# Kernel optimization log

Hardware: AMD Instinct MI355X
Metric: run time of the kernel (lower is better)

Reference implementation:

```python
import jax, jax.numpy as jnp
import numpy as np

D = 768

def _linear_params(key, name_idx, d_in, d_out):
    k1, k2 = jax.random.split(jax.random.fold_in(jax.random.key(42), name_idx))
    bound = 1.0 / np.sqrt(d_in)
    W = jax.random.uniform(k1, (d_out, d_in), jnp.float32, -bound, bound)
    b = jax.random.uniform(k2, (d_out,), jnp.float32, -bound, bound)
    return W, b

def setup_inputs() -> dict:
    key = jax.random.key(0)
    kq, kk, kv = jax.random.split(key, 3)
    B, S = 8, 2048
    inp = {
        'query': jax.random.normal(kq, (B, S, D), jnp.float32),
        'key': jax.random.normal(kk, (B, S, D), jnp.float32),
        'value': jax.random.normal(kv, (B, S, D), jnp.float32),
    }
    Wq, bq = _linear_params(key, 0, D, D)
    Wk, bk = _linear_params(key, 1, D, D)
    Wv, bv = _linear_params(key, 2, D, D)
    Wg1, bg1 = _linear_params(key, 3, D, D)
    Wg2, bg2 = _linear_params(key, 4, D, D)
    inp.update(Wq=Wq, bq=bq, Wk=Wk, bk=bk, Wv=Wv, bv=bv,
               Wg1=Wg1, bg1=bg1, Wg2=Wg2, bg2=bg2,
               text_scale=jnp.ones((1, D), jnp.float32))
    return inp

def reference(query, key, value, Wq, bq, Wk, bk, Wv, bv, Wg1, bg1, Wg2, bg2, text_scale):
    # Linear projections (torch Linear: x @ W.T + b)
    q = jnp.einsum('bsd,ed->bse', query, Wq) + bq
    k = jnp.einsum('bsd,ed->bse', key, Wk) + bk
    v = jnp.einsum('bsd,ed->bse', value, Wv) + bv
    scale = 1.0 / jnp.sqrt(jnp.float32(k.shape[-1]))
    scores = jnp.einsum('bqd,bkd->bqk', q, k) * scale  # [B, S, S]
    attn = jax.nn.softmax(scores, axis=-1)
    attended = jnp.einsum('bqk,bkd->bqd', attn, v)  # dropout = identity (eval)
    # text_gate: Linear -> ReLU -> Linear -> Sigmoid, then sigmoid applied AGAIN (faithful)
    h = jax.nn.relu(jnp.einsum('bsd,ed->bse', attended, Wg1) + bg1)
    gate = jax.nn.sigmoid(jnp.einsum('bsd,ed->bse', h, Wg2) + bg2)
    gated = jax.nn.sigmoid(gate) * attended * text_scale
    return gated
```

## Files before the change

kernel.cpp:

```cpp
#include <hip/hip_runtime.h>

typedef unsigned short ushort_t;
typedef __bf16 bf16x8 __attribute__((ext_vector_type(8)));
typedef float f32x4 __attribute__((ext_vector_type(4)));
typedef short short8 __attribute__((ext_vector_type(8)));

#define SBAR()   asm volatile("s_barrier" ::: "memory")
#define WAITV0() asm volatile("s_waitcnt vmcnt(0)" ::: "memory")
#define WAITV4() asm volatile("s_waitcnt vmcnt(4)" ::: "memory")
#define WAITV8() asm volatile("s_waitcnt vmcnt(8)" ::: "memory")

__device__ __forceinline__ float bf2f(unsigned short u) {
    union { unsigned int i; float f; } v; v.i = ((unsigned int)u) << 16; return v.f;
}
__device__ __forceinline__ unsigned short f2bf(float f) {
    union { float f; unsigned int i; } v; v.f = f;
    unsigned int r = v.i + 0x7fffu + ((v.i >> 16) & 1u);
    return (unsigned short)(r >> 16);
}
__device__ __forceinline__ float sigm(float x) { return 1.0f / (1.0f + __expf(-x)); }

__device__ __forceinline__ void async_copy16(const ushort_t* src, ushort_t* dst_lds) {
    __builtin_amdgcn_global_load_lds(
        (const __attribute__((address_space(1))) void*)src,
        (__attribute__((address_space(3))) void*)dst_lds,
        16, 0, 0);
}

#define WSEG 589824
#define NWALL 2949120
#define NTOT 2953728
__global__ __launch_bounds__(256)
void convert_params(const float* __restrict__ Wq, const float* __restrict__ Wk,
                    const float* __restrict__ Wv, const float* __restrict__ Wg1,
                    const float* __restrict__ Wg2, const float* __restrict__ bq,
                    const float* __restrict__ bk, const float* __restrict__ bv,
                    const float* __restrict__ bg1, const float* __restrict__ bg2,
                    const float* __restrict__ ts, ushort_t* __restrict__ dst)
{
    int i = (blockIdx.x * 256 + threadIdx.x) * 8;
    if (i >= NTOT) return;
    const float* src; int off;
    if (i < NWALL) {
        int wi = i / WSEG; off = i - wi * WSEG;
        src = (wi == 0) ? Wq : (wi == 1) ? Wk : (wi == 2) ? Wv : (wi == 3) ? Wg1 : Wg2;
    } else {
        int j = i - NWALL; int bi = j / 768; off = j - bi * 768;
        src = (bi == 0) ? bq : (bi == 1) ? bk : (bi == 2) ? bv : (bi == 3) ? bg1 : (bi == 4) ? bg2 : ts;
    }
    float4 a = *(const float4*)(src + off);
    float4 b = *(const float4*)(src + off + 4);
    short8 o;
    o[0] = (short)f2bf(a.x); o[1] = (short)f2bf(a.y); o[2] = (short)f2bf(a.z); o[3] = (short)f2bf(a.w);
    o[4] = (short)f2bf(b.x); o[5] = (short)f2bf(b.y); o[6] = (short)f2bf(b.z); o[7] = (short)f2bf(b.w);
    *(short8*)(dst + i) = o;
}

#define PERT 12582912ll
__global__ __launch_bounds__(256)
void convert_inputs(const float* __restrict__ q, const float* __restrict__ k,
                    const float* __restrict__ v, ushort_t* __restrict__ X)
{
    long long i = ((long long)blockIdx.x * 256 + threadIdx.x) * 8;
    const float* src; long long off;
    if (i < PERT)          { src = q; off = i; }
    else if (i < 2 * PERT) { src = k; off = i - PERT; }
    else                   { src = v; off = i - 2 * PERT; }
    float4 a = *(const float4*)(src + off);
    float4 b = *(const float4*)(src + off + 4);
    short8 o;
    o[0] = (short)f2bf(a.x); o[1] = (short)f2bf(a.y); o[2] = (short)f2bf(a.z); o[3] = (short)f2bf(a.w);
    o[4] = (short)f2bf(b.x); o[5] = (short)f2bf(b.y); o[6] = (short)f2bf(b.z); o[7] = (short)f2bf(b.w);
    *(short8*)(X + i) = o;
}

__global__ __launch_bounds__(256)
void finalize_rinv(const float* __restrict__ psums, float* __restrict__ rinv, int nb)
{
    int row = blockIdx.x * 256 + threadIdx.x;
    const float* p = psums + (size_t)row * nb;
    float s = 0.f;
    for (int i = 0; i < nb; ++i) s += p[i];
    rinv[row] = 1.0f / s;
}

template<int EPI, int CF32, int QKV>
__global__ __launch_bounds__(256, 2)
void gemm_bt(const ushort_t* __restrict__ A, const ushort_t* __restrict__ B,
             void* __restrict__ Cv, void* __restrict__ Cv2,
             const ushort_t* __restrict__ bias,
             const ushort_t* __restrict__ aux, const ushort_t* __restrict__ ts,
             const float* __restrict__ rinvg, float* __restrict__ psum_out,
             int M, int N, int K, float scale,
             long long batchA, long long batchB, long long batchC)
{
    __shared__ __align__(16) ushort_t As[3][128 * 32];
    __shared__ __align__(16) ushort_t Bs[3][128 * 32];
    __shared__ float rsmx[256];
    const int tid  = threadIdx.x;
    const int lane = tid & 63;
    const int wave = tid >> 6;
    const int wr = wave >> 1, wc = wave & 1;

    const int gx = gridDim.x, gy = gridDim.y;
    const int nwg = gx * gy * gridDim.z;
    int fid = (blockIdx.z * gy + blockIdx.y) * gx + blockIdx.x;
    fid = (fid & 7) * (nwg >> 3) + (fid >> 3);
    const int bz  = fid / (gx * gy);
    const int rem = fid - bz * (gx * gy);
    const int by  = rem / gx;
    const int bx  = rem - by * gx;
    const int row0 = by * 128;
    const int col0 = bx * 128;

    f32x4 acc[4][4] = {};

    const int srow = tid >> 2;
    const int scol = (tid & 3) * 8;
    const ushort_t* ga0 = A + batchA * bz + (size_t)(row0 + srow) * K + scol;
    const ushort_t* gb0 = B + batchB * bz + (size_t)(col0 + srow) * K + scol;

    const int kop  = (lane >> 4) * 8;
    const int arow = wr * 64 + (lane & 15);
    const int brow = wc * 64 + (lane & 15);

    const int NT = K >> 5;

#define STAGE4(T, BUF) do { const int kk_ = (T) * 32; \
    async_copy16(ga0 + kk_,                  &As[BUF][0] + tid * 8); \
    async_copy16(ga0 + (size_t)64 * K + kk_, &As[BUF][0] + 2048 + tid * 8); \
    async_copy16(gb0 + kk_,                  &Bs[BUF][0] + tid * 8); \
    async_copy16(gb0 + (size_t)64 * K + kk_, &Bs[BUF][0] + 2048 + tid * 8); \
} while (0)

    STAGE4(0, 0);
    STAGE4(1, 1);

    int cur = 0;
    for (int t = 0; t < NT; ++t) {
        if (t + 2 < NT) {
            int nb = cur + 2; if (nb >= 3) nb -= 3;
            STAGE4(t + 2, nb);
            WAITV8();
        } else if (t + 1 < NT) {
            WAITV4();
        } else {
            WAITV0();
        }
        SBAR();
        const ushort_t* Ac = &As[0][0] + cur * 4096;
        const ushort_t* Bc = &Bs[0][0] + cur * 4096;
        bf16x8 af[4], bfr[4];
        #pragma unroll
        for (int m = 0; m < 4; ++m)
            af[m] = *(const bf16x8*)(Ac + (arow + m * 16) * 32 + kop);
        #pragma unroll
        for (int n = 0; n < 4; ++n)
            bfr[n] = *(const bf16x8*)(Bc + (brow + n * 16) * 32 + kop);
        #pragma unroll
        for (int m = 0; m < 4; ++m)
            #pragma unroll
            for (int n = 0; n < 4; ++n)
                acc[m][n] = __builtin_amdgcn_mfma_f32_16x16x32_bf16(af[m], bfr[n], acc[m][n], 0, 0, 0);
        SBAR();
        ++cur; if (cur >= 3) cur = 0;
    }
#undef STAGE4

    const int r0 = row0 + wr * 64 + (lane >> 4) * 4;
    const int c0 = col0 + wc * 64 + (lane & 15);

    float rv[4][4];
    if (EPI == 7) {
        #pragma unroll
        for (int m = 0; m < 4; ++m)
            #pragma unroll
            for (int r = 0; r < 4; ++r)
                rv[m][r] = rinvg[(size_t)bz * M + r0 + m * 16 + r];
    }
    float rsum[4][4] = {};

    ushort_t* Cb = (QKV && bz == 2) ? (ushort_t*)Cv2 : (ushort_t*)Cv + batchC * bz;
    float* Cf = (float*)Cv;
    #pragma unroll
    for (int m = 0; m < 4; ++m) {
        #pragma unroll
        for (int n = 0; n < 4; ++n) {
            const int col = c0 + n * 16;
            #pragma unroll
            for (int r = 0; r < 4; ++r) {
                const int row = r0 + m * 16 + r;
                float val = acc[m][n][r];
                if (EPI == 1) {
                    val += bf2f(bias[(QKV ? bz * 768 : 0) + col]);
                } else if (EPI == 3) {
                    val += bf2f(bias[col]);
                    val = fmaxf(val, 0.0f);
                } else if (EPI == 4) {
                    val += bf2f(bias[col]);
                    float g  = sigm(val);
                    float gg = sigm(g);
                    val = gg * bf2f(aux[(size_t)row * N + col]) * bf2f(ts[col]);
                } else if (EPI == 5) {
                    val = __expf(val * scale);
                    rsum[m][r] += val;
                } else if (EPI == 7) {
                    val *= rv[m][r];
                }
                if (CF32) Cf[(size_t)row * N + col] = val;
                else      Cb[(size_t)row * N + col] = f2bf(val);
            }
        }
    }

    if (EPI == 5) {
        #pragma unroll
        for (int m = 0; m < 4; ++m)
            #pragma unroll
            for (int r = 0; r < 4; ++r) {
                float s = rsum[m][r];
                s += __shfl_xor(s, 1);
                s += __shfl_xor(s, 2);
                s += __shfl_xor(s, 4);
                s += __shfl_xor(s, 8);
                rsum[m][r] = s;
            }
        if ((lane & 15) == 0) {
            const int quad = lane >> 4;
            #pragma unroll
            for (int m = 0; m < 4; ++m)
                #pragma unroll
                for (int r = 0; r < 4; ++r)
                    rsmx[(wr * 64 + m * 16 + quad * 4 + r) * 2 + wc] = rsum[m][r];
        }
        __syncthreads();
        if (tid < 128) {
            float s = rsmx[tid * 2] + rsmx[tid * 2 + 1];
            psum_out[((size_t)bz * M + row0 + tid) * gx + bx] = s;
        }
    }
}

__global__ __launch_bounds__(256)
void transpose2d(const ushort_t* __restrict__ V, ushort_t* __restrict__ VT, int R, int Ccols)
{
    __shared__ ushort_t t[32][33];
    const size_t zoff = (size_t)blockIdx.z * R * Ccols;
    const int tx = threadIdx.x, ty = threadIdx.y;
    const int c = blockIdx.x * 32 + tx;
    const int rbase = blockIdx.y * 32;
    #pragma unroll
    for (int i = 0; i < 4; ++i)
        t[ty + i * 8][tx] = V[zoff + (size_t)(rbase + ty + i * 8) * Ccols + c];
    __syncthreads();
    const int r = rbase + tx;
    const int cbase = blockIdx.x * 32;
    #pragma unroll
    for (int i = 0; i < 4; ++i)
        VT[zoff + (size_t)(cbase + ty + i * 8) * R + r] = t[tx][ty + i * 8];
}

extern "C" void kernel_launch(void* const* d_in, const int* in_sizes, int n_in,
                              void* d_out, int out_size, void* d_ws, size_t ws_size,
                              hipStream_t stream)
{
    (void)in_sizes; (void)n_in; (void)out_size; (void)ws_size;
    const float* query = (const float*)d_in[0];
    const float* key_  = (const float*)d_in[1];
    const float* value = (const float*)d_in[2];
    const float* Wq  = (const float*)d_in[3];
    const float* bq  = (const float*)d_in[4];
    const float* Wk  = (const float*)d_in[5];
    const float* bk  = (const float*)d_in[6];
    const float* Wv  = (const float*)d_in[7];
    const float* bv  = (const float*)d_in[8];
    const float* Wg1 = (const float*)d_in[9];
    const float* bg1 = (const float*)d_in[10];
    const float* Wg2 = (const float*)d_in[11];
    const float* bg2 = (const float*)d_in[12];
    const float* tsc = (const float*)d_in[13];

    const int S = 2048, D = 768, Bc = 8;
    const int MS = Bc * S;
    const long long SD = (long long)S * D;
    const long long SS = (long long)S * S;
    const long long MSD = (long long)MS * D;

    char* ws = (char*)d_ws;
    ushort_t* q    = (ushort_t*)(ws);
    ushort_t* att  = q;
    ushort_t* k    = (ushort_t*)(ws + 25165824ll);
    float*    rinv = (float*)(ws + 25165824ll);
    ushort_t* h    = k;
    ushort_t* vT   = (ushort_t*)(ws + 50331648ll);
    ushort_t* X    = (ushort_t*)(ws + 50331648ll);
    ushort_t* P    = (ushort_t*)(ws + 75497472ll);
    ushort_t* Wb   = (ushort_t*)(ws + 142606336ll);
    ushort_t* v    = (ushort_t*)d_out;
    float*  psums  = (float*)d_out;

    const int WQ = 0, WG1 = 1769472, WG2 = 2359296;
    const int BQ = 2949120, BG1 = 2951424, BG2 = 2952192, TSO = 2952960;

    const dim3 blk(256);
    const float scale = 0.03608439182435161f;

    convert_params<<<dim3((NTOT / 8 + 255) / 256), blk, 0, stream>>>(
        Wq, Wk, Wv, Wg1, Wg2, bq, bk, bv, bg1, bg2, tsc, Wb);
    convert_inputs<<<dim3(18432), blk, 0, stream>>>(query, key_, value, X);
    gemm_bt<1, 0, 1><<<dim3(D / 128, MS / 128, 3), blk, 0, stream>>>(
        X, Wb + WQ, q, v, Wb + BQ, nullptr, nullptr, nullptr, nullptr,
        MS, D, D, 1.f, MSD, (long long)WSEG, MSD);
    transpose2d<<<dim3(D / 32, S / 32, Bc), dim3(32, 8), 0, stream>>>(v, vT, S, D);
    gemm_bt<5, 0, 0><<<dim3(S / 128, S / 128, Bc), blk, 0, stream>>>(
        q, k, P, nullptr, nullptr, nullptr, nullptr, nullptr, psums,
        S, S, D, scale, SD, SD, SS);
    finalize_rinv<<<dim3(MS / 256), blk, 0, stream>>>(psums, rinv, S / 128);
    gemm_bt<7, 0, 0><<<dim3(D / 128, S / 128, Bc), blk, 0, stream>>>(
        P, vT, att, nullptr, nullptr, nullptr, nullptr, rinv, nullptr,
        S, D, S, 1.f, SS, SD, SD);
    gemm_bt<3, 0, 0><<<dim3(D / 128, MS / 128, 1), blk, 0, stream>>>(
        att, Wb + WG1, h, nullptr, Wb + BG1, nullptr, nullptr, nullptr, nullptr,
        MS, D, D, 1.f, 0, 0, 0);
    gemm_bt<4, 1, 0><<<dim3(D / 128, MS / 128, 1), blk, 0, stream>>>(
        h, Wb + WG2, d_out, nullptr, Wb + BG2, att, Wb + TSO, nullptr, nullptr,
        MS, D, D, 1.f, 0, 0, 0);
}
```

Baseline: 332.3 us.

## Fuse fp32-to-bf16 input conversion into QKV projection GEMM A-tile loading

Removes the separate convert_inputs kernel. The QKV GEMM now reads fp32 query/key/value directly, converts them to bf16 in registers and writes them into a double-buffered LDS A tile, while B tiles keep using async LDS copies. This avoids writing and re-reading a 75MB bf16 intermediate, at the cost of a more serialized A-load path with register prefetch and extra barriers. The float-to-bf16 conversion also switches to hardware casts.

```diff
diff --git a/kernel.cpp b/kernel.cpp
--- a/kernel.cpp
+++ b/kernel.cpp
@@ -8,7 +8,9 @@
 #define SBAR()   asm volatile("s_barrier" ::: "memory")
 #define WAITV0() asm volatile("s_waitcnt vmcnt(0)" ::: "memory")
 #define WAITV4() asm volatile("s_waitcnt vmcnt(4)" ::: "memory")
+#define WAITV6() asm volatile("s_waitcnt vmcnt(6)" ::: "memory")
 #define WAITV8() asm volatile("s_waitcnt vmcnt(8)" ::: "memory")
+#define WAITL0() asm volatile("s_waitcnt lgkmcnt(0)" ::: "memory")
 
 __device__ __forceinline__ float bf2f(unsigned short u) {
     union { unsigned int i; float f; } v; v.i = ((unsigned int)u) << 16; return v.f;
@@ -25,6 +27,13 @@
         (const __attribute__((address_space(1))) void*)src,
         (__attribute__((address_space(3))) void*)dst_lds,
         16, 0, 0);
+}
+
+__device__ __forceinline__ short8 cvt8(float4 x, float4 y) {
+    bf16x8 h;
+    h[0] = (__bf16)x.x; h[1] = (__bf16)x.y; h[2] = (__bf16)x.z; h[3] = (__bf16)x.w;
+    h[4] = (__bf16)y.x; h[5] = (__bf16)y.y; h[6] = (__bf16)y.z; h[7] = (__bf16)y.w;
+    return __builtin_bit_cast(short8, h);
 }
 
 #define WSEG 589824
@@ -50,28 +59,7 @@
     }
     float4 a = *(const float4*)(src + off);
     float4 b = *(const float4*)(src + off + 4);
-    short8 o;
-    o[0] = (short)f2bf(a.x); o[1] = (short)f2bf(a.y); o[2] = (short)f2bf(a.z); o[3] = (short)f2bf(a.w);
-    o[4] = (short)f2bf(b.x); o[5] = (short)f2bf(b.y); o[6] = (short)f2bf(b.z); o[7] = (short)f2bf(b.w);
-    *(short8*)(dst + i) = o;
-}
-
-#define PERT 12582912ll
-__global__ __launch_bounds__(256)
-void convert_inputs(const float* __restrict__ q, const float* __restrict__ k,
-                    const float* __restrict__ v, ushort_t* __restrict__ X)
-{
-    long long i = ((long long)blockIdx.x * 256 + threadIdx.x) * 8;
-    const float* src; long long off;
-    if (i < PERT)          { src = q; off = i; }
-    else if (i < 2 * PERT) { src = k; off = i - PERT; }
-    else                   { src = v; off = i - 2 * PERT; }
-    float4 a = *(const float4*)(src + off);
-    float4 b = *(const float4*)(src + off + 4);
-    short8 o;
-    o[0] = (short)f2bf(a.x); o[1] = (short)f2bf(a.y); o[2] = (short)f2bf(a.z); o[3] = (short)f2bf(a.w);
-    o[4] = (short)f2bf(b.x); o[5] = (short)f2bf(b.y); o[6] = (short)f2bf(b.z); o[7] = (short)f2bf(b.w);
-    *(short8*)(X + i) = o;
+    *(short8*)(dst + i) = cvt8(a, b);
 }
 
 __global__ __launch_bounds__(256)
@@ -84,9 +72,10 @@
     rinv[row] = 1.0f / s;
 }
 
-template<int EPI, int CF32, int QKV>
+template<int EPI, int CF32, int QKV, int AF32>
 __global__ __launch_bounds__(256, 2)
-void gemm_bt(const ushort_t* __restrict__ A, const ushort_t* __restrict__ B,
+void gemm_bt(const void* __restrict__ Av, const void* __restrict__ Af1,
+             const void* __restrict__ Af2, const ushort_t* __restrict__ B,
              void* __restrict__ Cv, void* __restrict__ Cv2,
              const ushort_t* __restrict__ bias,
              const ushort_t* __restrict__ aux, const ushort_t* __restrict__ ts,
@@ -117,7 +106,7 @@
 
     const int srow = tid >> 2;
     const int scol = (tid & 3) * 8;
-    const ushort_t* ga0 = A + batchA * bz + (size_t)(row0 + srow) * K + scol;
+    const ushort_t* ga0 = (const ushort_t*)Av + batchA * bz + (size_t)(row0 + srow) * K + scol;
     const ushort_t* gb0 = B + batchB * bz + (size_t)(col0 + srow) * K + scol;
 
     const int kop  = (lane >> 4) * 8;
@@ -126,6 +115,70 @@
 
     const int NT = K >> 5;
 
+#define MFMA_STEP(AC, BC) do { \
+    bf16x8 af_[4], bf_[4]; \
+    _Pragma("unroll") \
+    for (int m = 0; m < 4; ++m) af_[m] = *(const bf16x8*)((AC) + (arow + m * 16) * 32 + kop); \
+    _Pragma("unroll") \
+    for (int n = 0; n < 4; ++n) bf_[n] = *(const bf16x8*)((BC) + (brow + n * 16) * 32 + kop); \
+    _Pragma("unroll") \
+    for (int m = 0; m < 4; ++m) \
+        _Pragma("unroll") \
+        for (int n = 0; n < 4; ++n) \
+            acc[m][n] = __builtin_amdgcn_mfma_f32_16x16x32_bf16(af_[m], bf_[n], acc[m][n], 0, 0, 0); \
+} while (0)
+
+    if (AF32) {
+        const float* gAf = (bz == 0) ? (const float*)Av : (bz == 1) ? (const float*)Af1
+                                                        : (const float*)Af2;
+        const float* gA  = gAf + (size_t)(row0 + srow) * K + scol;
+        const float* gA2 = gA + (size_t)64 * K;
+
+#define STAGEB2(T, BUF) do { const int kk_ = (T) * 32; \
+    async_copy16(gb0 + kk_,                  &Bs[BUF][0] + tid * 8); \
+    async_copy16(gb0 + (size_t)64 * K + kk_, &Bs[BUF][0] + 2048 + tid * 8); } while (0)
+
+        STAGEB2(0, 0);
+        STAGEB2(1, 1);
+        float4 pa0 = *(const float4*)(gA);      float4 pa1 = *(const float4*)(gA + 4);
+        float4 pa2 = *(const float4*)(gA2);     float4 pa3 = *(const float4*)(gA2 + 4);
+        float4 qa0, qa1, qa2, qa3;
+
+        for (int t = 0; t < NT; t += 2) {
+            if (t + 2 < NT) STAGEB2(t + 2, (t + 2) % 3);
+            if (t + 1 < NT) {
+                const int k1 = (t + 1) * 32;
+                qa0 = *(const float4*)(gA + k1);  qa1 = *(const float4*)(gA + k1 + 4);
+                qa2 = *(const float4*)(gA2 + k1); qa3 = *(const float4*)(gA2 + k1 + 4);
+            }
+            if (t + 2 < NT)      WAITV6();
+            else if (t + 1 < NT) WAITV4();
+            else                 WAITV0();
+            *(short8*)(&As[0][0] + tid * 8)        = cvt8(pa0, pa1);
+            *(short8*)(&As[0][0] + 2048 + tid * 8) = cvt8(pa2, pa3);
+            WAITL0();
+            SBAR();
+            MFMA_STEP(&As[0][0], &Bs[0][0] + (t % 3) * 4096);
+            SBAR();
+            const int t1 = t + 1;
+            if (t1 + 2 < NT) STAGEB2(t1 + 2, (t1 + 2) % 3);
+            if (t1 + 1 < NT) {
+                const int k1 = (t1 + 1) * 32;
+                pa0 = *(const float4*)(gA + k1);  pa1 = *(const float4*)(gA + k1 + 4);
+                pa2 = *(const float4*)(gA2 + k1); pa3 = *(const float4*)(gA2 + k1 + 4);
+            }
+            if (t1 + 2 < NT)      WAITV6();
+            else if (t1 + 1 < NT) WAITV4();
+            else                  WAITV0();
+            *(short8*)(&As[1][0] + tid * 8)        = cvt8(qa0, qa1);
+            *(short8*)(&As[1][0] + 2048 + tid * 8) = cvt8(qa2, qa3);
+            WAITL0();
+            SBAR();
+            MFMA_STEP(&As[1][0], &Bs[0][0] + (t1 % 3) * 4096);
+            SBAR();
+        }
+#undef STAGEB2
+    } else {
 #define STAGE4(T, BUF) do { const int kk_ = (T) * 32; \
     async_copy16(ga0 + kk_,                  &As[BUF][0] + tid * 8); \
     async_copy16(ga0 + (size_t)64 * K + kk_, &As[BUF][0] + 2048 + tid * 8); \
@@ -133,39 +186,28 @@
     async_copy16(gb0 + (size_t)64 * K + kk_, &Bs[BUF][0] + 2048 + tid * 8); \
 } while (0)
 
-    STAGE4(0, 0);
-    STAGE4(1, 1);
-
-    int cur = 0;
-    for (int t = 0; t < NT; ++t) {
-        if (t + 2 < NT) {
-            int nb = cur + 2; if (nb >= 3) nb -= 3;
-            STAGE4(t + 2, nb);
-            WAITV8();
-        } else if (t + 1 < NT) {
-            WAITV4();
-        } else {
-            WAITV0();
-        }
-        SBAR();
-        const ushort_t* Ac = &As[0][0] + cur * 4096;
-        const ushort_t* Bc = &Bs[0][0] + cur * 4096;
-        bf16x8 af[4], bfr[4];
-        #pragma unroll
-        for (int m = 0; m < 4; ++m)
-            af[m] = *(const bf16x8*)(Ac + (arow + m * 16) * 32 + kop);
-        #pragma unroll
-        for (int n = 0; n < 4; ++n)
-            bfr[n] = *(const bf16x8*)(Bc + (brow + n * 16) * 32 + kop);
-        #pragma unroll
-        for (int m = 0; m < 4; ++m)
-            #pragma unroll
-            for (int n = 0; n < 4; ++n)
-                acc[m][n] = __builtin_amdgcn_mfma_f32_16x16x32_bf16(af[m], bfr[n], acc[m][n], 0, 0, 0);
-        SBAR();
-        ++cur; if (cur >= 3) cur = 0;
-    }
+        STAGE4(0, 0);
+        STAGE4(1, 1);
+
+        int cur = 0;
+        for (int t = 0; t < NT; ++t) {
+            if (t + 2 < NT) {
+                int nb = cur + 2; if (nb >= 3) nb -= 3;
+                STAGE4(t + 2, nb);
+                WAITV8();
+            } else if (t + 1 < NT) {
+                WAITV4();
+            } else {
+                WAITV0();
+            }
+            SBAR();
+            MFMA_STEP(&As[0][0] + cur * 4096, &Bs[0][0] + cur * 4096);
+            SBAR();
+            ++cur; if (cur >= 3) cur = 0;
+        }
 #undef STAGE4
+    }
+#undef MFMA_STEP
 
     const int r0 = row0 + wr * 64 + (lane >> 4) * 4;
     const int c0 = col0 + wc * 64 + (lane & 15);
@@ -293,7 +335,6 @@
     float*    rinv = (float*)(ws + 25165824ll);
     ushort_t* h    = k;
     ushort_t* vT   = (ushort_t*)(ws + 50331648ll);
-    ushort_t* X    = (ushort_t*)(ws + 50331648ll);
     ushort_t* P    = (ushort_t*)(ws + 75497472ll);
     ushort_t* Wb   = (ushort_t*)(ws + 142606336ll);
     ushort_t* v    = (ushort_t*)d_out;
@@ -307,22 +348,21 @@
 
     convert_params<<<dim3((NTOT / 8 + 255) / 256), blk, 0, stream>>>(
         Wq, Wk, Wv, Wg1, Wg2, bq, bk, bv, bg1, bg2, tsc, Wb);
-    convert_inputs<<<dim3(18432), blk, 0, stream>>>(query, key_, value, X);
-    gemm_bt<1, 0, 1><<<dim3(D / 128, MS / 128, 3), blk, 0, stream>>>(
-        X, Wb + WQ, q, v, Wb + BQ, nullptr, nullptr, nullptr, nullptr,
-        MS, D, D, 1.f, MSD, (long long)WSEG, MSD);
+    gemm_bt<1, 0, 1, 1><<<dim3(D / 128, MS / 128, 3), blk, 0, stream>>>(
+        query, key_, value, Wb + WQ, q, v, Wb + BQ, nullptr, nullptr, nullptr, nullptr,
+        MS, D, D, 1.f, 0, (long long)WSEG, MSD);
     transpose2d<<<dim3(D / 32, S / 32, Bc), dim3(32, 8), 0, stream>>>(v, vT, S, D);
-    gemm_bt<5, 0, 0><<<dim3(S / 128, S / 128, Bc), blk, 0, stream>>>(
-        q, k, P, nullptr, nullptr, nullptr, nullptr, nullptr, psums,
+    gemm_bt<5, 0, 0, 0><<<dim3(S / 128, S / 128, Bc), blk, 0, stream>>>(
+        q, nullptr, nullptr, k, P, nullptr, nullptr, nullptr, nullptr, nullptr, psums,
         S, S, D, scale, SD, SD, SS);
     finalize_rinv<<<dim3(MS / 256), blk, 0, stream>>>(psums, rinv, S / 128);
-    gemm_bt<7, 0, 0><<<dim3(D / 128, S / 128, Bc), blk, 0, stream>>>(
-        P, vT, att, nullptr, nullptr, nullptr, nullptr, rinv, nullptr,
+    gemm_bt<7, 0, 0, 0><<<dim3(D / 128, S / 128, Bc), blk, 0, stream>>>(
+        P, nullptr, nullptr, vT, att, nullptr, nullptr, nullptr, nullptr, rinv, nullptr,
         S, D, S, 1.f, SS, SD, SD);
-    gemm_bt<3, 0, 0><<<dim3(D / 128, MS / 128, 1), blk, 0, stream>>>(
-        att, Wb + WG1, h, nullptr, Wb + BG1, nullptr, nullptr, nullptr, nullptr,
+    gemm_bt<3, 0, 0, 0><<<dim3(D / 128, MS / 128, 1), blk, 0, stream>>>(
+        att, nullptr, nullptr, Wb + WG1, h, nullptr, Wb + BG1, nullptr, nullptr, nullptr, nullptr,
         MS, D, D, 1.f, 0, 0, 0);
-    gemm_bt<4, 1, 0><<<dim3(D / 128, MS / 128, 1), blk, 0, stream>>>(
-        h, Wb + WG2, d_out, nullptr, Wb + BG2, att, Wb + TSO, nullptr, nullptr,
+    gemm_bt<4, 1, 0, 0><<<dim3(D / 128, MS / 128, 1), blk, 0, stream>>>(
+        h, nullptr, nullptr, Wb + WG2, d_out, nullptr, Wb + BG2, att, Wb + TSO, nullptr, nullptr,
         MS, D, D, 1.f, 0, 0, 0);
 }
```

After: 336.5 us. About the same (+1.3%).
